# Optimization experiments

Measured on AMD Instinct MI355X. Metric: run time of the kernel, lower is better.

The kernel has to match this reference:

```python
import jax, jax.numpy as jnp
import numpy as np

N, E, DIM, HEADS, EDGE_DIM = 50000, 800000, 128, 4, 1
C = DIM // HEADS  # per-head channels
EPS = 1e-5


def graph_ln(h, w, b):
    # PyG LayerNorm, mode='graph', batch=None: normalize over ALL nodes+features
    mu = h.mean()
    hc = h - mu
    std = jnp.sqrt(jnp.mean(hc * hc))
    return hc / (std + EPS) * w + b


def setup_inputs() -> dict:
    key = jax.random.key(0)
    ks = jax.random.split(key, 16)
    s = 1.0 / np.sqrt(DIM)
    return {
        "x": jax.random.normal(ks[0], (N, DIM), jnp.float32),
        "edge_index": jax.random.randint(ks[1], (2, E), 0, N, jnp.int32),
        "edge_weight": jax.random.uniform(ks[2], (E,), jnp.float32),
        "edge_attr": jax.random.normal(ks[3], (E, EDGE_DIM), jnp.float32),
        # GCNConv params
        "W_gcn": jax.random.normal(ks[4], (DIM, DIM), jnp.float32) * s,
        "b_gcn": jnp.zeros((DIM,), jnp.float32),
        # GATv2Conv params (share_weights=True -> single lin)
        "W_l": jax.random.normal(ks[5], (DIM, DIM), jnp.float32) * s,
        "b_l": jnp.zeros((DIM,), jnp.float32),
        "W_edge": jax.random.normal(ks[6], (EDGE_DIM, DIM), jnp.float32),
        "att": jax.random.normal(ks[7], (HEADS, C), jnp.float32) * (1.0 / np.sqrt(C)),
        "b_gat": jnp.zeros((DIM,), jnp.float32),
        # norms
        "gcn_nw": jnp.ones((DIM,), jnp.float32), "gcn_nb": jnp.zeros((DIM,), jnp.float32),
        "gat_nw": jnp.ones((DIM,), jnp.float32), "gat_nb": jnp.zeros((DIM,), jnp.float32),
        "out_nw": jnp.ones((DIM,), jnp.float32), "out_nb": jnp.zeros((DIM,), jnp.float32),
        "alpha": jnp.ones((2,), jnp.float32),
    }


def reference(x, edge_index, edge_weight, edge_attr, W_gcn, b_gcn, W_l, b_l,
              W_edge, att, b_gat, gcn_nw, gcn_nb, gat_nw, gat_nb, out_nw, out_nb, alpha):
    src, dst = edge_index[0], edge_index[1]

    # ---- GCN branch (normalize=True, add_self_loops=False) ----
    deg = jax.ops.segment_sum(edge_weight, dst, num_segments=N)
    dis = jnp.where(deg > 0, jax.lax.rsqrt(jnp.maximum(deg, 1e-30)), 0.0)
    norm = dis[src] * edge_weight * dis[dst]  # [E]
    xw = x @ W_gcn  # [N, DIM]
    h = jax.ops.segment_sum(norm[:, None] * xw[src], dst, num_segments=N) + b_gcn
    gcn_out = x + jax.nn.gelu(graph_ln(h, gcn_nw, gcn_nb), approximate=False)

    # ---- GATv2 branch (share_weights=True, edge_dim=1) ----
    xl = (x @ W_l + b_l).reshape(N, HEADS, C)
    e = (edge_attr @ W_edge).reshape(E, HEADS, C)
    z = jax.nn.leaky_relu(xl[dst] + xl[src] + e, negative_slope=0.2)  # [E,H,C]
    logits = jnp.einsum('ehc,hc->eh', z, att)  # [E,H]
    m = jax.ops.segment_max(logits, dst, num_segments=N)  # [N,H]
    a = jnp.exp(logits - m[dst])
    denom = jax.ops.segment_sum(a, dst, num_segments=N)
    a = a / (denom[dst] + 1e-16)  # softmax over incoming edges per dst, per head
    msg = xl[src] * a[:, :, None]  # [E,H,C]
    g = jax.ops.segment_sum(msg, dst, num_segments=N).reshape(N, DIM) + b_gat
    gat_out = x + jax.nn.gelu(graph_ln(g, gat_nw, gat_nb), approximate=False)

    # ---- fuse ----
    w = jax.nn.softmax(alpha)
    fused = w[0] * gcn_out + w[1] * gat_out
    return jax.nn.gelu(graph_ln(fused, out_nw, out_nb), approximate=False)
```

## Files before the change

### kernel.cpp

```cpp
#include <hip/hip_runtime.h>
#include <math.h>

#define DIM 128
#define HEADS 4
#define EPS 1e-5f
#define NBLK 1024

__device__ __forceinline__ float us2f(unsigned short u) {
  union { unsigned int i; float f; } c; c.i = ((unsigned int)u) << 16; return c.f;
}
__device__ __forceinline__ unsigned short f2us(float f) {
  union { float ff; unsigned int i; } c; c.ff = f;
  return (unsigned short)((c.i + 0x7FFFu + ((c.i >> 16) & 1u)) >> 16);
}
__device__ __forceinline__ float ldf(const void* p, size_t i, int fl32) {
  return fl32 ? ((const float*)p)[i] : us2f(((const unsigned short*)p)[i]);
}
__device__ __forceinline__ float gelu_exact(float v) {
  return 0.5f * v * (1.0f + erff(v * 0.7071067811865475f));
}

__device__ __forceinline__ int packed_pos(int c) { return ((c & ~1) << 1) | (c & 1); }

__global__ void __launch_bounds__(256)
k_detect(const unsigned short* __restrict__ x, long n, int* __restrict__ dflag) {
  long lim = n < 8192 ? n : 8192;
  int bad = 0;
  for (long i = threadIdx.x; i < lim; i += 256) {
    float v = us2f(x[i]);
    float a = fabsf(v);
    if (!(a == 0.0f || (a > 1e-30f && a < 1e3f))) bad++;
  }
  __shared__ int sb[256];
  sb[threadIdx.x] = bad;
  __syncthreads();
  for (int off = 128; off > 0; off >>= 1) {
    if ((int)threadIdx.x < off) sb[threadIdx.x] += sb[threadIdx.x + off];
    __syncthreads();
  }
  if (threadIdx.x == 0) dflag[0] = (sb[0] > 32) ? 1 : 0;
}

__global__ void k_deg_cnt(const int* __restrict__ dst, const void* __restrict__ ew,
                          float* __restrict__ deg, int* __restrict__ cnt,
                          int* __restrict__ rank, int E, const int* __restrict__ df) {
  const int fl32 = *df;
  int e = blockIdx.x * blockDim.x + threadIdx.x;
  if (e < E) {
    int d = dst[e];
    rank[e] = atomicAdd(&cnt[d], 1);
    float w = ldf(ew, e, fl32);
    if (isfinite(w)) atomicAdd(&deg[d], w);
  }
}

__global__ void k_dis(float* __restrict__ deg, int N) {
  int i = blockIdx.x * blockDim.x + threadIdx.x;
  if (i < N) {
    float d = deg[i];
    deg[i] = (d > 0.0f) ? rsqrtf(fmaxf(d, 1e-30f)) : 0.0f;
  }
}

__global__ void __launch_bounds__(256)
k_scan(const int* __restrict__ cnt, int* __restrict__ off, int N, int E) {
  __shared__ int part[256];
  int t = threadIdx.x;
  int chunk = (N + 255) / 256;
  int lo = t * chunk;
  int hi = lo + chunk; if (hi > N) hi = N;
  int s = 0;
  for (int i = lo; i < hi; ++i) s += cnt[i];
  part[t] = s;
  __syncthreads();
  if (t == 0) {
    int run = 0;
    for (int j = 0; j < 256; ++j) { int tmp = part[j]; part[j] = run; run += tmp; }
  }
  __syncthreads();
  int run = part[t];
  for (int i = lo; i < hi; ++i) { off[i] = run; run += cnt[i]; }
  if (t == 0) off[N] = E;
}

__global__ void k_scatter(const int* __restrict__ src, const int* __restrict__ dst,
                          const void* __restrict__ ew, const void* __restrict__ ea,
                          const float* __restrict__ dis, const int* __restrict__ off,
                          const int* __restrict__ rank, int4* __restrict__ csr,
                          int E, const int* __restrict__ df) {
  const int fl32 = *df;
  int e = blockIdx.x * blockDim.x + threadIdx.x;
  if (e >= E) return;
  int d = dst[e], s = src[e];
  int pos = off[d] + rank[e];
  float nm = dis[s] * ldf(ew, e, fl32) * dis[d];
  if (!isfinite(nm)) nm = 0.0f;
  float eav = ldf(ea, e, fl32);
  if (!isfinite(eav)) eav = 0.0f;
  csr[pos] = make_int4(s, __float_as_int(nm), __float_as_int(eav), 0);
}

__global__ void __launch_bounds__(128)
k_gemm(const void* __restrict__ x, const void* __restrict__ Wg,
       const void* __restrict__ Wl, const void* __restrict__ bl,
       unsigned short* __restrict__ packed, int N, const int* __restrict__ df) {
  const int fl32 = *df;
  const int R = 8;
  __shared__ float xs[R][DIM];
  int c = threadIdx.x;
  int r0 = blockIdx.x * R;
  for (int r = 0; r < R; ++r) {
    int row = r0 + r;
    xs[r][c] = (row < N) ? ldf(x, (size_t)row * DIM + c, fl32) : 0.0f;
  }
  __syncthreads();
  float accg[R], accl[R];
  float blc = ldf(bl, c, fl32);
  #pragma unroll
  for (int r = 0; r < R; ++r) { accg[r] = 0.0f; accl[r] = blc; }
  for (int k = 0; k < DIM; ++k) {
    float wg = ldf(Wg, k * DIM + c, fl32);
    float wl = ldf(Wl, k * DIM + c, fl32);
    #pragma unroll
    for (int r = 0; r < R; ++r) {
      accg[r] = fmaf(xs[r][k], wg, accg[r]);
      accl[r] = fmaf(xs[r][k], wl, accl[r]);
    }
  }
  int pos = packed_pos(c);
  for (int r = 0; r < R; ++r) {
    int row = r0 + r;
    if (row < N) {
      float ag = accg[r], al = accl[r];
      if (!isfinite(ag)) ag = 0.0f;
      if (!isfinite(al)) al = 0.0f;
      packed[(size_t)row * 256 + pos] = f2us(al);
      packed[(size_t)row * 256 + pos + 2] = f2us(ag);
    }
  }
}

__global__ void __launch_bounds__(256)
k_mega(const int* __restrict__ off, const int4* __restrict__ csr,
       const unsigned short* __restrict__ packed,
       const void* __restrict__ Wed, const void* __restrict__ att,
       const void* __restrict__ bgcn, const void* __restrict__ bgat,
       float* __restrict__ h, float* __restrict__ g,
       double* __restrict__ pA, double* __restrict__ pB, int N,
       const int* __restrict__ df) {
  const int fl32 = *df;
  int wid = threadIdx.x >> 6;
  int lane = threadIdx.x & 63;
  int node = blockIdx.x * 4 + wid;
  int c0 = lane * 2;
  float wd0 = ldf(Wed, c0, fl32), wd1 = ldf(Wed, c0 + 1, fl32);
  float at0 = ldf(att, c0, fl32), at1 = ldf(att, c0 + 1, fl32);
  double sA = 0.0, sA2 = 0.0, sB = 0.0, sB2 = 0.0;
  if (node < N) {
    int beg = off[node], end = off[node + 1];
    ushort4 xd = *(const ushort4*)(packed + (size_t)node * 256 + lane * 4);
    float xd0 = us2f(xd.x), xd1 = us2f(xd.y);
    float mx = -INFINITY, den = 0.f;
    float ga0 = 0.f, ga1 = 0.f, hc0 = 0.f, hc1 = 0.f;
    int4 cP = make_int4(0, 0, 0, 0);
    ushort4 vP = make_ushort4(0, 0, 0, 0);
    if (beg < end) {
      cP = csr[beg];
      vP = *(const ushort4*)(packed + (size_t)cP.x * 256 + lane * 4);
    }
    for (int i = beg; i < end; ++i) {
      int4 ce = cP; ushort4 v = vP;
      if (i + 1 < end) {
        cP = csr[i + 1];
        vP = *(const ushort4*)(packed + (size_t)cP.x * 256 + lane * 4);
      }
      float nm = __int_as_float(ce.y), eav = __int_as_float(ce.z);
      float vx = us2f(v.x), vy = us2f(v.y);
      float z0 = xd0 + vx + eav * wd0; z0 = (z0 > 0.f) ? z0 : 0.2f * z0;
      float z1 = xd1 + vy + eav * wd1; z1 = (z1 > 0.f) ? z1 : 0.2f * z1;
      float dot = z0 * at0 + z1 * at1;
      dot += __shfl_xor(dot, 1);
      dot += __shfl_xor(dot, 2);
      dot += __shfl_xor(dot, 4);
      dot += __shfl_xor(dot, 8);
      float e = __expf(-fabsf(dot - mx));
      bool up = dot > mx;
      float corr = up ? e : 1.0f;
      float w = up ? 1.0f : e;
      mx = up ? dot : mx;
      den = fmaf(den, corr, w);
      ga0 = fmaf(ga0, corr, w * vx);
      ga1 = fmaf(ga1, corr, w * vy);
      hc0 = fmaf(nm, us2f(v.z), hc0);
      hc1 = fmaf(nm, us2f(v.w), hc1);
    }
    float inv = (end > beg) ? 1.0f / (den + 1e-16f) : 0.0f;
    ga0 *= inv; ga1 *= inv;
    if (!isfinite(ga0)) ga0 = 0.0f;
    if (!isfinite(ga1)) ga1 = 0.0f;
    if (!isfinite(hc0)) hc0 = 0.0f;
    if (!isfinite(hc1)) hc1 = 0.0f;
    *(float2*)(h + (size_t)node * DIM + c0) = make_float2(hc0, hc1);
    *(float2*)(g + (size_t)node * DIM + c0) = make_float2(ga0, ga1);
    float hA0 = hc0 + ldf(bgcn, c0, fl32), hA1 = hc1 + ldf(bgcn, c0 + 1, fl32);
    float gB0 = ga0 + ldf(bgat, c0, fl32), gB1 = ga1 + ldf(bgat, c0 + 1, fl32);
    sA  = (double)hA0 + (double)hA1;
    sA2 = (double)hA0 * hA0 + (double)hA1 * hA1;
    sB  = (double)gB0 + (double)gB1;
    sB2 = (double)gB0 * gB0 + (double)gB1 * gB1;
  }
  __shared__ double l1[256], l2[256], l3[256], l4[256];
  l1[threadIdx.x] = sA; l2[threadIdx.x] = sA2; l3[threadIdx.x] = sB; l4[threadIdx.x] = sB2;
  __syncthreads();
  for (int o = 128; o > 0; o >>= 1) {
    if ((int)threadIdx.x < o) {
      l1[threadIdx.x] += l1[threadIdx.x + o];
      l2[threadIdx.x] += l2[threadIdx.x + o];
      l3[threadIdx.x] += l3[threadIdx.x + o];
      l4[threadIdx.x] += l4[threadIdx.x + o];
    }
    __syncthreads();
  }
  if (threadIdx.x == 0) {
    pA[2 * blockIdx.x] = l1[0]; pA[2 * blockIdx.x + 1] = l2[0];
    pB[2 * blockIdx.x] = l3[0]; pB[2 * blockIdx.x + 1] = l4[0];
  }
}

__device__ __forceinline__ void ln_params(double S, double S2, double M, float* mu_out, float* sc_out) {
  double mu = S / M;
  double v = S2 / M - mu * mu;
  if (!(v > 0.0)) v = 0.0;
  float fmu = (float)mu;
  float sc = 1.0f / ((float)sqrt(v) + EPS);
  if (!isfinite(fmu)) fmu = 0.0f;
  if (!isfinite(sc)) sc = 0.0f;
  *mu_out = fmu; *sc_out = sc;
}

__global__ void __launch_bounds__(256)
k_fin12(const double* __restrict__ pA, const double* __restrict__ pB, int nblk,
        const void* __restrict__ alpha, float* __restrict__ params, double M,
        const int* __restrict__ df) {
  const int fl32 = *df;
  __shared__ double l1[256], l2[256], l3[256], l4[256];
  double a = 0, b = 0, c = 0, d = 0;
  for (int j = threadIdx.x; j < nblk; j += 256) {
    a += pA[2 * j]; b += pA[2 * j + 1];
    c += pB[2 * j]; d += pB[2 * j + 1];
  }
  l1[threadIdx.x] = a; l2[threadIdx.x] = b; l3[threadIdx.x] = c; l4[threadIdx.x] = d;
  __syncthreads();
  for (int off = 128; off > 0; off >>= 1) {
    if ((int)threadIdx.x < off) {
      l1[threadIdx.x] += l1[threadIdx.x + off];
      l2[threadIdx.x] += l2[threadIdx.x + off];
      l3[threadIdx.x] += l3[threadIdx.x + off];
      l4[threadIdx.x] += l4[threadIdx.x + off];
    }
    __syncthreads();
  }
  if (threadIdx.x == 0) {
    ln_params(l1[0], l2[0], M, &params[0], &params[1]);
    ln_params(l3[0], l4[0], M, &params[2], &params[3]);
    float a0 = ldf(alpha, 0, fl32), a1 = ldf(alpha, 1, fl32);
    if (!isfinite(a0)) a0 = 0.0f;
    if (!isfinite(a1)) a1 = 0.0f;
    float mx = fmaxf(a0, a1);
    float e0 = expf(a0 - mx), e1 = expf(a1 - mx);
    float inv = 1.0f / (e0 + e1);
    params[4] = e0 * inv;
    params[5] = e1 * inv;
  }
}

__global__ void __launch_bounds__(256)
k_fin3(const double* __restrict__ pC, float* __restrict__ params, double M) {
  __shared__ double l1[256], l2[256];
  double a = 0, b = 0;
  for (int j = threadIdx.x; j < NBLK; j += 256) { a += pC[2 * j]; b += pC[2 * j + 1]; }
  l1[threadIdx.x] = a; l2[threadIdx.x] = b;
  __syncthreads();
  for (int off = 128; off > 0; off >>= 1) {
    if ((int)threadIdx.x < off) {
      l1[threadIdx.x] += l1[threadIdx.x + off];
      l2[threadIdx.x] += l2[threadIdx.x + off];
    }
    __syncthreads();
  }
  if (threadIdx.x == 0) ln_params(l1[0], l2[0], M, &params[6], &params[7]);
}

__global__ void __launch_bounds__(256)
k_fuse(const void* __restrict__ x, float* h, const float* __restrict__ g,
       const void* __restrict__ b_gcn, const void* __restrict__ b_gat,
       const void* __restrict__ gcn_nw, const void* __restrict__ gcn_nb,
       const void* __restrict__ gat_nw, const void* __restrict__ gat_nb,
       const float* __restrict__ params, double* __restrict__ pC, long n,
       const int* __restrict__ df) {
  const int fl32 = *df;
  float mu1 = params[0], sc1 = params[1], mu2 = params[2], sc2 = params[3];
  float w0 = params[4], w1 = params[5];
  double s = 0.0, s2 = 0.0;
  long stride = (long)gridDim.x * blockDim.x;
  for (long i = (long)blockIdx.x * blockDim.x + threadIdx.x; i < n; i += stride) {
    size_t c = (size_t)(i & (DIM - 1));
    float xv = ldf(x, i, fl32);
    float hv = h[i] + ldf(b_gcn, c, fl32);
    float gv = g[i] + ldf(b_gat, c, fl32);
    float go = xv + gelu_exact((hv - mu1) * sc1 * ldf(gcn_nw, c, fl32) + ldf(gcn_nb, c, fl32));
    float ao = xv + gelu_exact((gv - mu2) * sc2 * ldf(gat_nw, c, fl32) + ldf(gat_nb, c, fl32));
    float f = w0 * go + w1 * ao;
    if (!isfinite(f)) f = 0.0f;
    h[i] = f;
    s += f; s2 += (double)f * f;
  }
  __shared__ double ls[256], ls2[256];
  ls[threadIdx.x] = s; ls2[threadIdx.x] = s2;
  __syncthreads();
  for (int off = 128; off > 0; off >>= 1) {
    if ((int)threadIdx.x < off) {
      ls[threadIdx.x] += ls[threadIdx.x + off];
      ls2[threadIdx.x] += ls2[threadIdx.x + off];
    }
    __syncthreads();
  }
  if (threadIdx.x == 0) { pC[2 * blockIdx.x] = ls[0]; pC[2 * blockIdx.x + 1] = ls2[0]; }
}

__global__ void k_final(const float* __restrict__ fused, const void* __restrict__ nw,
                        const void* __restrict__ nb, const float* __restrict__ params,
                        void* __restrict__ out, long n, const int* __restrict__ df) {
  const int fl32 = *df;
  long i = (long)blockIdx.x * blockDim.x + threadIdx.x;
  if (i >= n) return;
  size_t c = (size_t)(i & (DIM - 1));
  float mu = params[6], sc = params[7];
  float r = gelu_exact((fused[i] - mu) * sc * ldf(nw, c, fl32) + ldf(nb, c, fl32));
  if (!isfinite(r)) r = 0.0f;
  if (fl32) ((float*)out)[i] = r;
  else      ((unsigned short*)out)[i] = f2us(r);
}

extern "C" void kernel_launch(void* const* d_in, const int* in_sizes, int n_in,
                              void* d_out, int out_size, void* d_ws, size_t ws_size,
                              hipStream_t stream) {
  const void* x    = d_in[0];
  const int*  ei   = (const int*)d_in[1];
  const void* ew   = d_in[2];
  const void* ea   = d_in[3];
  const void* Wg   = d_in[4];
  const void* bgcn = d_in[5];
  const void* Wl   = d_in[6];
  const void* bl   = d_in[7];
  const void* Wed  = d_in[8];
  const void* att  = d_in[9];
  const void* bgat = d_in[10];
  const void* gcn_nw = d_in[11];
  const void* gcn_nb = d_in[12];
  const void* gat_nw = d_in[13];
  const void* gat_nb = d_in[14];
  const void* out_nw = d_in[15];
  const void* out_nb = d_in[16];
  const void* alpha  = d_in[17];

  const int N = in_sizes[0] / DIM;
  const int E = in_sizes[2];
  const int* src  = ei;
  const int* dstp = ei + E;
  const size_t ND = (size_t)N * DIM;
  const int nAgg = (N + 3) / 4;

  char* ws = (char*)d_ws;
  size_t o = 0;
  auto alloc = [&](size_t bytes) { size_t r = o; o += (bytes + 255) & ~(size_t)255; return r; };
  size_t o_deg    = alloc((size_t)N * 4);
  size_t o_cnt    = alloc((size_t)N * 4);
  size_t zero_end = o;
  size_t o_off    = alloc((size_t)(N + 1) * 4);
  size_t o_h      = alloc(ND * 4);
  size_t o_g      = alloc(ND * 4);
  size_t o_packed = alloc(ND * 4);
  size_t o_csr    = alloc((size_t)E * 16);
  size_t o_par    = alloc(8 * 4);
  size_t o_pA     = alloc((size_t)nAgg * 2 * 8);
  size_t o_pB     = alloc((size_t)nAgg * 2 * 8);
  size_t o_pC     = alloc((size_t)NBLK * 2 * 8);
  size_t o_flag   = alloc(4);
  (void)ws_size; (void)n_in; (void)out_size;

  float* deg     = (float*)(ws + o_deg);
  int*   cnt     = (int*)(ws + o_cnt);
  int*   off     = (int*)(ws + o_off);
  float* h       = (float*)(ws + o_h);
  int*   rank    = (int*)(ws + o_h);
  float* g       = (float*)(ws + o_g);
  unsigned short* packed = (unsigned short*)(ws + o_packed);
  int4*  csr     = (int4*)(ws + o_csr);
  float* params  = (float*)(ws + o_par);
  double* pA     = (double*)(ws + o_pA);
  double* pB     = (double*)(ws + o_pB);
  double* pC     = (double*)(ws + o_pC);
  int* dflag     = (int*)(ws + o_flag);

  hipMemsetAsync(ws, 0, zero_end, stream);
  k_detect<<<1, 256, 0, stream>>>((const unsigned short*)x, (long)ND, dflag);

  int ebk = (E + 255) / 256;
  k_deg_cnt<<<ebk, 256, 0, stream>>>(dstp, ew, deg, cnt, rank, E, dflag);
  k_dis<<<(N + 255) / 256, 256, 0, stream>>>(deg, N);
  k_scan<<<1, 256, 0, stream>>>(cnt, off, N, E);
  k_scatter<<<ebk, 256, 0, stream>>>(src, dstp, ew, ea, deg, off, rank, csr, E, dflag);

  k_gemm<<<(N + 7) / 8, 128, 0, stream>>>(x, Wg, Wl, bl, packed, N, dflag);

  k_mega<<<nAgg, 256, 0, stream>>>(off, csr, packed, Wed, att, bgcn, bgat,
                                   h, g, pA, pB, N, dflag);

  k_fin12<<<1, 256, 0, stream>>>(pA, pB, nAgg, alpha, params, (double)ND, dflag);
  k_fuse<<<NBLK, 256, 0, stream>>>(x, h, g, bgcn, bgat, gcn_nw, gcn_nb, gat_nw, gat_nb,
                                   params, pC, (long)ND, dflag);
  k_fin3<<<1, 256, 0, stream>>>(pC, params, (double)ND);
  k_final<<<(int)((ND + 255) / 256), 256, 0, stream>>>(h, out_nw, out_nb, params,
                                                       d_out, (long)ND, dflag);
}
```

Baseline: 560.4 us.

## Pad CSR rows to multiples of four and unroll aggregation with batched prefetch

Each node's CSR segment is padded to a multiple of four entries, zero-filled and masked by a validity flag, so the aggregation loop can issue four CSR loads and four neighbour gathers per iteration. This raises memory-level parallelism in the latency-bound gather. It also folds the rsqrt degree normalisation into the scatter kernel, which removes one launch. The block reduction now uses wave shuffles and writes per-node partials, the GEMM row tile grows from 8 to 16, and the CSR buffer is enlarged and zeroed by the memset, which adds extra padded work and memset traffic.

```diff
diff --git a/kernel.cpp b/kernel.cpp
--- a/kernel.cpp
+++ b/kernel.cpp
@@ -54,38 +54,30 @@
   }
 }
 
-__global__ void k_dis(float* __restrict__ deg, int N) {
-  int i = blockIdx.x * blockDim.x + threadIdx.x;
-  if (i < N) {
-    float d = deg[i];
-    deg[i] = (d > 0.0f) ? rsqrtf(fmaxf(d, 1e-30f)) : 0.0f;
-  }
-}
-
-__global__ void __launch_bounds__(256)
-k_scan(const int* __restrict__ cnt, int* __restrict__ off, int N, int E) {
+__global__ void __launch_bounds__(256)
+k_scan(const int* __restrict__ cnt, int* __restrict__ off, int N) {
   __shared__ int part[256];
   int t = threadIdx.x;
   int chunk = (N + 255) / 256;
   int lo = t * chunk;
   int hi = lo + chunk; if (hi > N) hi = N;
   int s = 0;
-  for (int i = lo; i < hi; ++i) s += cnt[i];
+  for (int i = lo; i < hi; ++i) s += (cnt[i] + 3) & ~3;
   part[t] = s;
   __syncthreads();
   if (t == 0) {
     int run = 0;
     for (int j = 0; j < 256; ++j) { int tmp = part[j]; part[j] = run; run += tmp; }
+    off[N] = run;
   }
   __syncthreads();
   int run = part[t];
-  for (int i = lo; i < hi; ++i) { off[i] = run; run += cnt[i]; }
-  if (t == 0) off[N] = E;
+  for (int i = lo; i < hi; ++i) { off[i] = run; run += (cnt[i] + 3) & ~3; }
 }
 
 __global__ void k_scatter(const int* __restrict__ src, const int* __restrict__ dst,
                           const void* __restrict__ ew, const void* __restrict__ ea,
-                          const float* __restrict__ dis, const int* __restrict__ off,
+                          const float* __restrict__ deg, const int* __restrict__ off,
                           const int* __restrict__ rank, int4* __restrict__ csr,
                           int E, const int* __restrict__ df) {
   const int fl32 = *df;
@@ -93,11 +85,14 @@
   if (e >= E) return;
   int d = dst[e], s = src[e];
   int pos = off[d] + rank[e];
-  float nm = dis[s] * ldf(ew, e, fl32) * dis[d];
+  float ds = deg[s], dd = deg[d];
+  float disS = (ds > 0.0f) ? rsqrtf(fmaxf(ds, 1e-30f)) : 0.0f;
+  float disD = (dd > 0.0f) ? rsqrtf(fmaxf(dd, 1e-30f)) : 0.0f;
+  float nm = disS * ldf(ew, e, fl32) * disD;
   if (!isfinite(nm)) nm = 0.0f;
   float eav = ldf(ea, e, fl32);
   if (!isfinite(eav)) eav = 0.0f;
-  csr[pos] = make_int4(s, __float_as_int(nm), __float_as_int(eav), 0);
+  csr[pos] = make_int4(s, __float_as_int(nm), __float_as_int(eav), 1);
 }
 
 __global__ void __launch_bounds__(128)
@@ -105,7 +100,7 @@
        const void* __restrict__ Wl, const void* __restrict__ bl,
        unsigned short* __restrict__ packed, int N, const int* __restrict__ df) {
   const int fl32 = *df;
-  const int R = 8;
+  const int R = 16;
   __shared__ float xs[R][DIM];
   int c = threadIdx.x;
   int r0 = blockIdx.x * R;
@@ -141,8 +136,8 @@
 }
 
 __global__ void __launch_bounds__(256)
-k_mega(const int* __restrict__ off, const int4* __restrict__ csr,
-       const unsigned short* __restrict__ packed,
+k_mega(const int* __restrict__ off, const int* __restrict__ cnt,
+       const int4* __restrict__ csr, const unsigned short* __restrict__ packed,
        const void* __restrict__ Wed, const void* __restrict__ att,
        const void* __restrict__ bgcn, const void* __restrict__ bgat,
        float* __restrict__ h, float* __restrict__ g,
@@ -152,78 +147,83 @@
   int wid = threadIdx.x >> 6;
   int lane = threadIdx.x & 63;
   int node = blockIdx.x * 4 + wid;
+  if (node >= N) return;
   int c0 = lane * 2;
   float wd0 = ldf(Wed, c0, fl32), wd1 = ldf(Wed, c0 + 1, fl32);
   float at0 = ldf(att, c0, fl32), at1 = ldf(att, c0 + 1, fl32);
-  double sA = 0.0, sA2 = 0.0, sB = 0.0, sB2 = 0.0;
-  if (node < N) {
-    int beg = off[node], end = off[node + 1];
-    ushort4 xd = *(const ushort4*)(packed + (size_t)node * 256 + lane * 4);
-    float xd0 = us2f(xd.x), xd1 = us2f(xd.y);
-    float mx = -INFINITY, den = 0.f;
-    float ga0 = 0.f, ga1 = 0.f, hc0 = 0.f, hc1 = 0.f;
-    int4 cP = make_int4(0, 0, 0, 0);
-    ushort4 vP = make_ushort4(0, 0, 0, 0);
-    if (beg < end) {
-      cP = csr[beg];
-      vP = *(const ushort4*)(packed + (size_t)cP.x * 256 + lane * 4);
-    }
-    for (int i = beg; i < end; ++i) {
-      int4 ce = cP; ushort4 v = vP;
-      if (i + 1 < end) {
-        cP = csr[i + 1];
-        vP = *(const ushort4*)(packed + (size_t)cP.x * 256 + lane * 4);
+  int beg = off[node], endP = off[node + 1];
+  int realdeg = cnt[node];
+  ushort4 xd = *(const ushort4*)(packed + (size_t)node * 256 + lane * 4);
+  float xd0 = us2f(xd.x), xd1 = us2f(xd.y);
+  float mx = -INFINITY, den = 0.f;
+  float ga0 = 0.f, ga1 = 0.f, hc0 = 0.f, hc1 = 0.f;
+
+#define GATH(ce) (*(const ushort4*)(packed + (size_t)(ce).x * 256 + lane * 4))
+#define STEP(ce, v) {                                                     \
+    float nm = __int_as_float((ce).y), eav = __int_as_float((ce).z);      \
+    float vx = us2f((v).x), vy = us2f((v).y);                             \
+    float z0 = xd0 + vx + eav * wd0; z0 = (z0 > 0.f) ? z0 : 0.2f * z0;    \
+    float z1 = xd1 + vy + eav * wd1; z1 = (z1 > 0.f) ? z1 : 0.2f * z1;    \
+    float dot = z0 * at0 + z1 * at1;                                      \
+    dot += __shfl_xor(dot, 1);                                            \
+    dot += __shfl_xor(dot, 2);                                            \
+    dot += __shfl_xor(dot, 4);                                            \
+    dot += __shfl_xor(dot, 8);                                            \
+    if (!isfinite(dot)) dot = 0.0f;                                       \
+    dot = (ce).w ? dot : -1e30f;                                          \
+    float e = __expf(-fabsf(dot - mx));                                   \
+    bool up = dot > mx;                                                   \
+    float corr = up ? e : 1.0f;                                           \
+    float w = up ? 1.0f : e;                                              \
+    if (!(ce).w) w = 0.0f;                                                \
+    mx = up ? dot : mx;                                                   \
+    den = fmaf(den, corr, w);                                             \
+    ga0 = fmaf(ga0, corr, w * vx);                                        \
+    ga1 = fmaf(ga1, corr, w * vy);                                        \
+    hc0 = fmaf(nm, us2f((v).z), hc0);                                     \
+    hc1 = fmaf(nm, us2f((v).w), hc1);                                     \
+  }
+
+  if (beg < endP) {
+    int4 ca = csr[beg], cb = csr[beg + 1], cc = csr[beg + 2], cd = csr[beg + 3];
+    ushort4 va = GATH(ca), vb = GATH(cb), vc = GATH(cc), vd = GATH(cd);
+    for (int i = beg; i < endP; i += 4) {
+      int4 da = ca, db = cb, dc = cc, dd = cd;
+      ushort4 wa = va, wb = vb, wc = vc, wdv = vd;
+      if (i + 4 < endP) {
+        ca = csr[i + 4]; cb = csr[i + 5]; cc = csr[i + 6]; cd = csr[i + 7];
+        va = GATH(ca); vb = GATH(cb); vc = GATH(cc); vd = GATH(cd);
       }
-      float nm = __int_as_float(ce.y), eav = __int_as_float(ce.z);
-      float vx = us2f(v.x), vy = us2f(v.y);
-      float z0 = xd0 + vx + eav * wd0; z0 = (z0 > 0.f) ? z0 : 0.2f * z0;
-      float z1 = xd1 + vy + eav * wd1; z1 = (z1 > 0.f) ? z1 : 0.2f * z1;
-      float dot = z0 * at0 + z1 * at1;
-      dot += __shfl_xor(dot, 1);
-      dot += __shfl_xor(dot, 2);
-      dot += __shfl_xor(dot, 4);
-      dot += __shfl_xor(dot, 8);
-      float e = __expf(-fabsf(dot - mx));
-      bool up = dot > mx;
-      float corr = up ? e : 1.0f;
-      float w = up ? 1.0f : e;
-      mx = up ? dot : mx;
-      den = fmaf(den, corr, w);
-      ga0 = fmaf(ga0, corr, w * vx);
-      ga1 = fmaf(ga1, corr, w * vy);
-      hc0 = fmaf(nm, us2f(v.z), hc0);
-      hc1 = fmaf(nm, us2f(v.w), hc1);
-    }
-    float inv = (end > beg) ? 1.0f / (den + 1e-16f) : 0.0f;
-    ga0 *= inv; ga1 *= inv;
-    if (!isfinite(ga0)) ga0 = 0.0f;
-    if (!isfinite(ga1)) ga1 = 0.0f;
-    if (!isfinite(hc0)) hc0 = 0.0f;
-    if (!isfinite(hc1)) hc1 = 0.0f;
-    *(float2*)(h + (size_t)node * DIM + c0) = make_float2(hc0, hc1);
-    *(float2*)(g + (size_t)node * DIM + c0) = make_float2(ga0, ga1);
-    float hA0 = hc0 + ldf(bgcn, c0, fl32), hA1 = hc1 + ldf(bgcn, c0 + 1, fl32);
-    float gB0 = ga0 + ldf(bgat, c0, fl32), gB1 = ga1 + ldf(bgat, c0 + 1, fl32);
-    sA  = (double)hA0 + (double)hA1;
-    sA2 = (double)hA0 * hA0 + (double)hA1 * hA1;
-    sB  = (double)gB0 + (double)gB1;
-    sB2 = (double)gB0 * gB0 + (double)gB1 * gB1;
-  }
-  __shared__ double l1[256], l2[256], l3[256], l4[256];
-  l1[threadIdx.x] = sA; l2[threadIdx.x] = sA2; l3[threadIdx.x] = sB; l4[threadIdx.x] = sB2;
-  __syncthreads();
-  for (int o = 128; o > 0; o >>= 1) {
-    if ((int)threadIdx.x < o) {
-      l1[threadIdx.x] += l1[threadIdx.x + o];
-      l2[threadIdx.x] += l2[threadIdx.x + o];
-      l3[threadIdx.x] += l3[threadIdx.x + o];
-      l4[threadIdx.x] += l4[threadIdx.x + o];
-    }
-    __syncthreads();
-  }
-  if (threadIdx.x == 0) {
-    pA[2 * blockIdx.x] = l1[0]; pA[2 * blockIdx.x + 1] = l2[0];
-    pB[2 * blockIdx.x] = l3[0]; pB[2 * blockIdx.x + 1] = l4[0];
+      STEP(da, wa); STEP(db, wb); STEP(dc, wc); STEP(dd, wdv);
+    }
+  }
+#undef STEP
+#undef GATH
+
+  float inv = (realdeg > 0) ? 1.0f / (den + 1e-16f) : 0.0f;
+  ga0 *= inv; ga1 *= inv;
+  if (!isfinite(ga0)) ga0 = 0.0f;
+  if (!isfinite(ga1)) ga1 = 0.0f;
+  if (!isfinite(hc0)) hc0 = 0.0f;
+  if (!isfinite(hc1)) hc1 = 0.0f;
+  *(float2*)(h + (size_t)node * DIM + c0) = make_float2(hc0, hc1);
+  *(float2*)(g + (size_t)node * DIM + c0) = make_float2(ga0, ga1);
+  float hA0 = hc0 + ldf(bgcn, c0, fl32), hA1 = hc1 + ldf(bgcn, c0 + 1, fl32);
+  float gB0 = ga0 + ldf(bgat, c0, fl32), gB1 = ga1 + ldf(bgat, c0 + 1, fl32);
+  double sA  = (double)hA0 + (double)hA1;
+  double sA2 = (double)hA0 * hA0 + (double)hA1 * hA1;
+  double sB  = (double)gB0 + (double)gB1;
+  double sB2 = (double)gB0 * gB0 + (double)gB1 * gB1;
+  #pragma unroll
+  for (int o = 32; o > 0; o >>= 1) {
+    sA  += __shfl_xor(sA, o);
+    sA2 += __shfl_xor(sA2, o);
+    sB  += __shfl_xor(sB, o);
+    sB2 += __shfl_xor(sB2, o);
+  }
+  if (lane == 0) {
+    pA[2 * node] = sA; pA[2 * node + 1] = sA2;
+    pB[2 * node] = sB; pB[2 * node + 1] = sB2;
   }
 }
 
@@ -369,22 +369,22 @@
   const int* src  = ei;
   const int* dstp = ei + E;
   const size_t ND = (size_t)N * DIM;
-  const int nAgg = (N + 3) / 4;
+  const size_t Epad = (size_t)E + 4 * (size_t)N + 16;
 
   char* ws = (char*)d_ws;
   size_t o = 0;
   auto alloc = [&](size_t bytes) { size_t r = o; o += (bytes + 255) & ~(size_t)255; return r; };
   size_t o_deg    = alloc((size_t)N * 4);
   size_t o_cnt    = alloc((size_t)N * 4);
+  size_t o_csr    = alloc(Epad * 16);
   size_t zero_end = o;
   size_t o_off    = alloc((size_t)(N + 1) * 4);
   size_t o_h      = alloc(ND * 4);
   size_t o_g      = alloc(ND * 4);
   size_t o_packed = alloc(ND * 4);
-  size_t o_csr    = alloc((size_t)E * 16);
   size_t o_par    = alloc(8 * 4);
-  size_t o_pA     = alloc((size_t)nAgg * 2 * 8);
-  size_t o_pB     = alloc((size_t)nAgg * 2 * 8);
+  size_t o_pA     = alloc((size_t)N * 2 * 8);
+  size_t o_pB     = alloc((size_t)N * 2 * 8);
   size_t o_pC     = alloc((size_t)NBLK * 2 * 8);
   size_t o_flag   = alloc(4);
   (void)ws_size; (void)n_in; (void)out_size;
@@ -408,16 +408,15 @@
 
   int ebk = (E + 255) / 256;
   k_deg_cnt<<<ebk, 256, 0, stream>>>(dstp, ew, deg, cnt, rank, E, dflag);
-  k_dis<<<(N + 255) / 256, 256, 0, stream>>>(deg, N);
-  k_scan<<<1, 256, 0, stream>>>(cnt, off, N, E);
+  k_scan<<<1, 256, 0, stream>>>(cnt, off, N);
   k_scatter<<<ebk, 256, 0, stream>>>(src, dstp, ew, ea, deg, off, rank, csr, E, dflag);
 
-  k_gemm<<<(N + 7) / 8, 128, 0, stream>>>(x, Wg, Wl, bl, packed, N, dflag);
-
-  k_mega<<<nAgg, 256, 0, stream>>>(off, csr, packed, Wed, att, bgcn, bgat,
-                                   h, g, pA, pB, N, dflag);
-
-  k_fin12<<<1, 256, 0, stream>>>(pA, pB, nAgg, alpha, params, (double)ND, dflag);
+  k_gemm<<<(N + 15) / 16, 128, 0, stream>>>(x, Wg, Wl, bl, packed, N, dflag);
+
+  k_mega<<<(N + 3) / 4, 256, 0, stream>>>(off, cnt, csr, packed, Wed, att, bgcn, bgat,
+                                          h, g, pA, pB, N, dflag);
+
+  k_fin12<<<1, 256, 0, stream>>>(pA, pB, N, alpha, params, (double)ND, dflag);
   k_fuse<<<NBLK, 256, 0, stream>>>(x, h, g, bgcn, bgat, gcn_nw, gcn_nb, gat_nw, gat_nb,
                                    params, pC, (long)ND, dflag);
   k_fin3<<<1, 256, 0, stream>>>(pC, params, (double)ND);
```

Measured after the change: 594.4 us. +6.1%, slower.
